# Kernel tuning notes

Measured on AMD Instinct MI355X. Metric: run time of the kernel, lower is better.

## Reference

```python
import jax, jax.numpy as jnp
import numpy as np

D_IN = 1024
D_OUT = 1024
B, S = 4, 2048

def setup_inputs() -> dict:
    key = jax.random.key(0)
    ks = jax.random.split(key, 7)
    s_in = 1.0 / np.sqrt(D_IN)
    return {
        "X": jax.random.normal(ks[0], (B, S, D_IN), dtype=jnp.float32),
        "Wq": jax.random.uniform(ks[1], (D_OUT, D_IN), jnp.float32, -s_in, s_in),
        "bq": jax.random.uniform(ks[2], (D_OUT,), jnp.float32, -s_in, s_in),
        "Wk": jax.random.uniform(ks[3], (D_OUT, D_IN), jnp.float32, -s_in, s_in),
        "bk": jax.random.uniform(ks[4], (D_OUT,), jnp.float32, -s_in, s_in),
        "Wv": jax.random.uniform(ks[5], (D_OUT, D_IN), jnp.float32, -s_in, s_in),
        "bv": jax.random.uniform(ks[6], (D_OUT,), jnp.float32, -s_in, s_in),
    }

def reference(X, Wq, bq, Wk, bk, Wv, bv):
    # Linear projections (torch Linear: x @ W.T + b)
    q = X @ Wq.T + bq            # [B, S, D_OUT]
    k = X @ Wk.T + bk
    v = X @ Wv.T + bv
    scores = jnp.einsum("bqd,bkd->bqk", q, k) / jnp.sqrt(jnp.float32(D_OUT))
    seq = scores.shape[-1]
    causal = jnp.tril(jnp.ones((seq, seq), dtype=bool))  # True where allowed
    scores = jnp.where(causal, scores, -jnp.inf)
    attn = jax.nn.softmax(scores, axis=-1)
    return jnp.einsum("bqk,bkd->bqd", attn, v)
```

## Files before the change

kernel.cpp:

```cpp
#include <hip/hip_runtime.h>
#include <hip/hip_bf16.h>
#include <hip/hip_fp8.h>


typedef __attribute__((ext_vector_type(8))) short short8;
typedef __attribute__((ext_vector_type(4))) float floatx4;
typedef __attribute__((ext_vector_type(2))) long longx2;

#define SEQ   2048
#define DMODEL 1024
#define NBATCH 4
#define MTOT  (SEQ * NBATCH)

__device__ __forceinline__ void stage16(const void* g, void* l)
{
  __builtin_amdgcn_global_load_lds(
      (const __attribute__((address_space(1))) void*)g,
      (__attribute__((address_space(3))) void*)l, 16, 0, 0);
}

__device__ __forceinline__ unsigned short bf16_bits(float f)
{
  __hip_bfloat16 h = __float2bfloat16(f);
  return *(unsigned short*)&h;
}

__device__ __forceinline__ unsigned char fp8_bits(float f)
{
  __hip_fp8_e4m3 h(f);
  return h.__x;
}

__global__ __launch_bounds__(256) void convert_all(
    const float* __restrict__ X,  const float* __restrict__ Wq,
    const float* __restrict__ Wk, const float* __restrict__ Wv,
    __hip_bfloat16* __restrict__ Xb,  __hip_bfloat16* __restrict__ Wqb,
    __hip_bfloat16* __restrict__ Wkb, __hip_bfloat16* __restrict__ Wvb)
{
  const int b = blockIdx.x;
  const float* src; __hip_bfloat16* dst; int rel;
  if (b < 8192)       { src = X;  dst = Xb;  rel = b; }
  else if (b < 9216)  { src = Wq; dst = Wqb; rel = b - 8192; }
  else if (b < 10240) { src = Wk; dst = Wkb; rel = b - 9216; }
  else                { src = Wv; dst = Wvb; rel = b - 10240; }
  const int i = rel * 1024 + threadIdx.x * 4;
  float4 f = *(const float4*)(src + i);
  uint2 o;
  o.x = (unsigned)bf16_bits(f.x) | ((unsigned)bf16_bits(f.y) << 16);
  o.y = (unsigned)bf16_bits(f.z) | ((unsigned)bf16_bits(f.w) << 16);
  *(uint2*)(dst + i) = o;
}

__global__ __launch_bounds__(256, 2) void gemm_qkv_fused(
    const __hip_bfloat16* __restrict__ Xb,
    const __hip_bfloat16* __restrict__ Wqb,
    const __hip_bfloat16* __restrict__ Wkb,
    const __hip_bfloat16* __restrict__ Wvb,
    const float* __restrict__ bq, const float* __restrict__ bk, const float* __restrict__ bv,
    unsigned char* __restrict__ Qb, unsigned char* __restrict__ Kb,
    __hip_bfloat16* __restrict__ Vt)
{
  __shared__ __hip_bfloat16 As[128 * 32];
  __shared__ __hip_bfloat16 Bs[3][128 * 32];
  const int m0 = blockIdx.y * 128, n0 = blockIdx.x * 128;
  const int tid  = threadIdx.x;
  const int lane = tid & 63;
  const int wave = tid >> 6;
  const int quad = lane >> 4;
  const int r    = lane & 15;
  const int wm   = (wave >> 1) * 64;
  const int wn   = (wave & 1) * 64;
  const int srow = wave * 16 + (lane >> 2);
  const int scol = (lane & 3) * 8;

  const __hip_bfloat16* Wp[3] = {Wqb, Wkb, Wvb};

  __hip_bfloat16* lA0 = As + wave * 512;
  __hip_bfloat16* lA1 = As + 2048 + wave * 512;

  const __hip_bfloat16* aR0 = Xb + (size_t)(m0 + srow) * DMODEL + scol;
  const __hip_bfloat16* aR1 = aR0 + (size_t)64 * DMODEL;

  floatx4 acc[3][4][4] = {};

  for (int kt = 0; kt < DMODEL / 32; ++kt) {
    const int k0 = kt * 32;
    stage16(aR0 + k0, lA0);
    stage16(aR1 + k0, lA1);
#pragma unroll
    for (int w = 0; w < 3; ++w) {
      stage16(Wp[w] + (size_t)(n0 + srow) * DMODEL + scol + k0,      Bs[w] + wave * 512);
      stage16(Wp[w] + (size_t)(n0 + 64 + srow) * DMODEL + scol + k0, Bs[w] + 2048 + wave * 512);
    }
    __syncthreads();
    short8 a[4];
#pragma unroll
    for (int i = 0; i < 4; ++i)
      a[i] = *(const short8*)(As + (wm + i * 16 + r) * 32 + quad * 8);
#pragma unroll
    for (int w = 0; w < 3; ++w) {
      short8 b[4];
#pragma unroll
      for (int j = 0; j < 4; ++j)
        b[j] = *(const short8*)(Bs[w] + (wn + j * 16 + r) * 32 + quad * 8);
#pragma unroll
      for (int i = 0; i < 4; ++i)
#pragma unroll
        for (int j = 0; j < 4; ++j)
          acc[w][i][j] = __builtin_amdgcn_mfma_f32_16x16x32_bf16(a[i], b[j], acc[w][i][j], 0, 0, 0);
    }
    __syncthreads();
  }

  {
    unsigned char* Op[2] = {Qb, Kb};
    const float* Bp[2] = {bq, bk};
#pragma unroll
    for (int w = 0; w < 2; ++w) {
      unsigned char* out = Op[w];
#pragma unroll
      for (int j = 0; j < 4; ++j) {
        const int n = n0 + wn + j * 16 + r;
        const float bb = Bp[w][n];
#pragma unroll
        for (int i = 0; i < 4; ++i) {
          const int mbase = m0 + wm + i * 16 + quad * 4;
#pragma unroll
          for (int e = 0; e < 4; ++e)
            out[(size_t)(mbase + e) * DMODEL + n] = fp8_bits(acc[w][i][j][e] + bb);
        }
      }
    }
  }
  {
    const int z    = m0 >> 11;
    const int posb = (m0 & (SEQ - 1)) + wm;
    __hip_bfloat16* vt = Vt + (size_t)z * DMODEL * SEQ;
#pragma unroll
    for (int j = 0; j < 4; ++j) {
      const int n = n0 + wn + j * 16 + r;
      const float bb = bv[n];
#pragma unroll
      for (int i = 0; i < 4; ++i) {
        const int pos = posb + i * 16 + quad * 4;
        unsigned long long pk =
            (unsigned long long)bf16_bits(acc[2][i][j][0] + bb)
          | ((unsigned long long)bf16_bits(acc[2][i][j][1] + bb) << 16)
          | ((unsigned long long)bf16_bits(acc[2][i][j][2] + bb) << 32)
          | ((unsigned long long)bf16_bits(acc[2][i][j][3] + bb) << 48);
        *(unsigned long long*)(vt + (size_t)n * SEQ + pos) = pk;
      }
    }
  }
}

__device__ __forceinline__ void gemm_core_2w_fp8(
    const unsigned char* __restrict__ A,
    const unsigned char* __restrict__ B,
    int K, int m0, int n0, int kchunks,
    unsigned char* As , unsigned char* Bs ,
    floatx4 acc[4][4])
{
  const int tid  = threadIdx.x;
  const int lane = tid & 63;
  const int wave = tid >> 6;
  const int quad = lane >> 4;
  const int r    = lane & 15;
  const int wn   = wave * 64;
  const int lrow = lane >> 2;
  const int lcol = (lane & 3) * 16;

  const unsigned char* aB = A + (size_t)(m0 + wave * 32 + lrow) * K + lcol;
  const unsigned char* bB = B + (size_t)(n0 + wave * 64 + lrow) * K + lcol;
  unsigned char* lA = As + wave * 2048;
  unsigned char* lB = Bs + wave * 4096;

  for (int kt = 0; kt < kchunks; ++kt) {
    const int k0 = kt * 64;
#pragma unroll
    for (int s = 0; s < 2; ++s)
      stage16(aB + (size_t)(16 * s) * K + k0, lA + s * 1024);
#pragma unroll
    for (int s = 0; s < 4; ++s)
      stage16(bB + (size_t)(16 * s) * K + k0, lB + s * 1024);
    __syncthreads();
    longx2 a[4], b[4];
#pragma unroll
    for (int i = 0; i < 4; ++i) {
      a[i] = __builtin_bit_cast(longx2, *(const int4*)(As + (i * 16 + r) * 64 + quad * 16));
      b[i] = __builtin_bit_cast(longx2, *(const int4*)(Bs + (wn + i * 16 + r) * 64 + quad * 16));
    }
#pragma unroll
    for (int kk = 0; kk < 2; ++kk)
#pragma unroll
      for (int i = 0; i < 4; ++i)
#pragma unroll
        for (int j = 0; j < 4; ++j)
          acc[i][j] = __builtin_amdgcn_mfma_f32_16x16x32_fp8_fp8(
              a[i][kk], b[j][kk], acc[i][j], 0, 0, 0);
    __syncthreads();
  }
}

template <bool SUMS>
__device__ __forceinline__ void gemm_core_2w(
    const __hip_bfloat16* __restrict__ A,
    const __hip_bfloat16* __restrict__ B,
    int K, int m0, int n0, int kchunks,
    __hip_bfloat16* As , __hip_bfloat16* Bs ,
    floatx4 acc[4][4], floatx4 acc_s[4])
{
  const int tid  = threadIdx.x;
  const int lane = tid & 63;
  const int wave = tid >> 6;
  const int quad = lane >> 4;
  const int r    = lane & 15;
  const int wn   = wave * 64;
  const int lrow = lane >> 2;
  const int lcol = (lane & 3) * 8;

  short8 ones;
#pragma unroll
  for (int t = 0; t < 8; ++t) ones[t] = (short)0x3F80;

  const __hip_bfloat16* aB = A + (size_t)(m0 + wave * 32 + lrow) * K + lcol;
  const __hip_bfloat16* bB = B + (size_t)(n0 + wave * 64 + lrow) * K + lcol;
  __hip_bfloat16* lA = As + wave * 1024;
  __hip_bfloat16* lB = Bs + wave * 2048;

  for (int kt = 0; kt < kchunks; ++kt) {
    const int k0 = kt * 32;
#pragma unroll
    for (int s = 0; s < 2; ++s)
      stage16(aB + (size_t)(16 * s) * K + k0, lA + s * 512);
#pragma unroll
    for (int s = 0; s < 4; ++s)
      stage16(bB + (size_t)(16 * s) * K + k0, lB + s * 512);
    __syncthreads();
    short8 a[4], b[4];
#pragma unroll
    for (int i = 0; i < 4; ++i) {
      a[i] = *(const short8*)(As + (i * 16 + r) * 32 + quad * 8);
      b[i] = *(const short8*)(Bs + (wn + i * 16 + r) * 32 + quad * 8);
    }
    if (SUMS) {
#pragma unroll
      for (int i = 0; i < 4; ++i)
        acc_s[i] = __builtin_amdgcn_mfma_f32_16x16x32_bf16(a[i], ones, acc_s[i], 0, 0, 0);
    }
#pragma unroll
    for (int i = 0; i < 4; ++i)
#pragma unroll
      for (int j = 0; j < 4; ++j)
        acc[i][j] = __builtin_amdgcn_mfma_f32_16x16x32_bf16(a[i], b[j], acc[i][j], 0, 0, 0);
    __syncthreads();
  }
}

__global__ __launch_bounds__(128, 4) void gemm_scores(
    const unsigned char* __restrict__ Qb, const unsigned char* __restrict__ Kb,
    __hip_bfloat16* __restrict__ Sb)
{
  const int z = blockIdx.y;
  const int L = blockIdx.x;
  int p = (int)((sqrtf(4.0f * (float)L + 1.0f) - 1.0f) * 0.5f);
  while ((p + 1) * (p + 2) <= L) ++p;
  while (p * (p + 1) > L) --p;
  const int o  = L - p * (p + 1);
  const int mt = 2 * p + (o > p ? 1 : 0);
  const int nt = (o > p) ? (o - p - 1) : o;
  const int m0 = mt * 64, n0 = nt * 128;

  __shared__ unsigned char As[64 * 64], Bs[128 * 64];
  const unsigned char* A = Qb + (size_t)z * SEQ * DMODEL;
  const unsigned char* B = Kb + (size_t)z * SEQ * DMODEL;
  __hip_bfloat16* outp = Sb + (size_t)z * SEQ * SEQ;
  floatx4 acc[4][4] = {};
  gemm_core_2w_fp8(A, B, DMODEL, m0, n0, DMODEL / 64, As, Bs, acc);

  const int lane = threadIdx.x & 63, wave = threadIdx.x >> 6;
  const int quad = lane >> 4, r = lane & 15;
  const int wn = wave * 64;
  const float scale = 0.03125f;
#pragma unroll
  for (int i = 0; i < 4; ++i) {
    const int mbase = m0 + i * 16 + quad * 4;
#pragma unroll
    for (int e = 0; e < 4; ++e) {
      const int row = mbase + e;
#pragma unroll
      for (int j = 0; j < 4; ++j) {
        const int n = n0 + wn + j * 16 + r;
        const float pv = (n <= row) ? __expf(acc[i][j][e] * scale) : 0.f;
        outp[(size_t)row * SEQ + n] = __float2bfloat16(pv);
      }
    }
  }
}

__global__ __launch_bounds__(128, 4) void gemm_pv(
    const __hip_bfloat16* __restrict__ Sb, const __hip_bfloat16* __restrict__ Vt,
    float* __restrict__ Out)
{
  __shared__ __hip_bfloat16 As[64 * 32], Bs[128 * 32];
  const int z = blockIdx.z;
  const int mt = (int)gridDim.y - 1 - (int)blockIdx.y;
  const int m0 = mt * 64, n0 = blockIdx.x * 128;
  const __hip_bfloat16* A = Sb + (size_t)z * SEQ * SEQ;
  const __hip_bfloat16* B = Vt + (size_t)z * DMODEL * SEQ;
  float* outp = Out + (size_t)z * SEQ * DMODEL;

  floatx4 acc[4][4] = {};
  floatx4 acc_s[4] = {};
  const int kchunks = 2 * mt + 2;
  gemm_core_2w<true>(A, B, SEQ, m0, n0, kchunks, As, Bs, acc, acc_s);

  const int lane = threadIdx.x & 63, wave = threadIdx.x >> 6;
  const int quad = lane >> 4, r = lane & 15;
  const int wn = wave * 64;
#pragma unroll
  for (int i = 0; i < 4; ++i) {
    const int mbase = m0 + i * 16 + quad * 4;
    float inv[4];
#pragma unroll
    for (int e = 0; e < 4; ++e) inv[e] = 1.f / acc_s[i][e];
#pragma unroll
    for (int j = 0; j < 4; ++j) {
      const int n = n0 + wn + j * 16 + r;
#pragma unroll
      for (int e = 0; e < 4; ++e)
        outp[(size_t)(mbase + e) * DMODEL + n] = acc[i][j][e] * inv[e];
    }
  }
}

extern "C" void kernel_launch(void* const* d_in, const int* in_sizes, int n_in,
                              void* d_out, int out_size, void* d_ws, size_t ws_size,
                              hipStream_t stream)
{
  const float* X  = (const float*)d_in[0];
  const float* Wq = (const float*)d_in[1];
  const float* bq = (const float*)d_in[2];
  const float* Wk = (const float*)d_in[3];
  const float* bk = (const float*)d_in[4];
  const float* Wv = (const float*)d_in[5];
  const float* bv = (const float*)d_in[6];
  float* Out = (float*)d_out;

  char* ws = (char*)d_ws;
  size_t off = 0;
  auto alloc = [&](size_t bytes) -> void* {
    void* p = ws + off;
    off += (bytes + 255) & ~(size_t)255;
    return p;
  };
  __hip_bfloat16* Xb  = (__hip_bfloat16*)alloc((size_t)MTOT * DMODEL * 2);
  __hip_bfloat16* Wqb = (__hip_bfloat16*)alloc((size_t)DMODEL * DMODEL * 2);
  __hip_bfloat16* Wkb = (__hip_bfloat16*)alloc((size_t)DMODEL * DMODEL * 2);
  __hip_bfloat16* Wvb = (__hip_bfloat16*)alloc((size_t)DMODEL * DMODEL * 2);
  unsigned char*  Qb  = (unsigned char*)alloc((size_t)MTOT * DMODEL);
  unsigned char*  Kb  = (unsigned char*)alloc((size_t)MTOT * DMODEL);
  __hip_bfloat16* Vt  = (__hip_bfloat16*)alloc((size_t)MTOT * DMODEL * 2);
  __hip_bfloat16* Sb  = (__hip_bfloat16*)alloc((size_t)NBATCH * SEQ * SEQ * 2);
  (void)ws_size; (void)in_sizes; (void)n_in; (void)out_size;

  convert_all<<<11264, 256, 0, stream>>>(X, Wq, Wk, Wv, Xb, Wqb, Wkb, Wvb);
  gemm_qkv_fused<<<dim3(DMODEL / 128, MTOT / 128), 256, 0, stream>>>(
      Xb, Wqb, Wkb, Wvb, bq, bk, bv, Qb, Kb, Vt);
  gemm_scores<<<dim3(272, NBATCH), 128, 0, stream>>>(Qb, Kb, Sb);
  gemm_pv<<<dim3(DMODEL / 128, SEQ / 64, NBATCH), 128, 0, stream>>>(Sb, Vt, Out);
}
```

Baseline: 235.6 us.

## Enlarge score and PV GEMM tiles to 128x128 with 4 waves and XCD-aware block mapping

The scores and PV GEMMs move from 64x128 tiles on 2 waves to 128x128 tiles on 4 waves arranged 2x2. This raises operand reuse per LDS load and halves the number of tile loads per output. Block indices are remapped so neighbouring work lands on the same XCD, which should improve L2 locality, and PV processes heavy rows first. The trade-off is coarser causal granularity, with more masked work on diagonal tiles, and fewer blocks for load balancing.

```diff
diff --git a/kernel.cpp b/kernel.cpp
--- a/kernel.cpp
+++ b/kernel.cpp
@@ -154,7 +154,7 @@
   }
 }
 
-__device__ __forceinline__ void gemm_core_2w_fp8(
+__device__ __forceinline__ void gemm_core_4w_fp8(
     const unsigned char* __restrict__ A,
     const unsigned char* __restrict__ B,
     int K, int m0, int n0, int kchunks,
@@ -166,28 +166,28 @@
   const int wave = tid >> 6;
   const int quad = lane >> 4;
   const int r    = lane & 15;
-  const int wn   = wave * 64;
+  const int wm   = (wave >> 1) * 64;
+  const int wn   = (wave & 1) * 64;
   const int lrow = lane >> 2;
   const int lcol = (lane & 3) * 16;
 
   const unsigned char* aB = A + (size_t)(m0 + wave * 32 + lrow) * K + lcol;
-  const unsigned char* bB = B + (size_t)(n0 + wave * 64 + lrow) * K + lcol;
+  const unsigned char* bB = B + (size_t)(n0 + wave * 32 + lrow) * K + lcol;
   unsigned char* lA = As + wave * 2048;
-  unsigned char* lB = Bs + wave * 4096;
+  unsigned char* lB = Bs + wave * 2048;
 
   for (int kt = 0; kt < kchunks; ++kt) {
     const int k0 = kt * 64;
 #pragma unroll
-    for (int s = 0; s < 2; ++s)
+    for (int s = 0; s < 2; ++s) {
       stage16(aB + (size_t)(16 * s) * K + k0, lA + s * 1024);
-#pragma unroll
-    for (int s = 0; s < 4; ++s)
       stage16(bB + (size_t)(16 * s) * K + k0, lB + s * 1024);
+    }
     __syncthreads();
     longx2 a[4], b[4];
 #pragma unroll
     for (int i = 0; i < 4; ++i) {
-      a[i] = __builtin_bit_cast(longx2, *(const int4*)(As + (i * 16 + r) * 64 + quad * 16));
+      a[i] = __builtin_bit_cast(longx2, *(const int4*)(As + (wm + i * 16 + r) * 64 + quad * 16));
       b[i] = __builtin_bit_cast(longx2, *(const int4*)(Bs + (wn + i * 16 + r) * 64 + quad * 16));
     }
 #pragma unroll
@@ -203,7 +203,7 @@
 }
 
 template <bool SUMS>
-__device__ __forceinline__ void gemm_core_2w(
+__device__ __forceinline__ void gemm_core_4w(
     const __hip_bfloat16* __restrict__ A,
     const __hip_bfloat16* __restrict__ B,
     int K, int m0, int n0, int kchunks,
@@ -215,7 +215,8 @@
   const int wave = tid >> 6;
   const int quad = lane >> 4;
   const int r    = lane & 15;
-  const int wn   = wave * 64;
+  const int wm   = (wave >> 1) * 64;
+  const int wn   = (wave & 1) * 64;
   const int lrow = lane >> 2;
   const int lcol = (lane & 3) * 8;
 
@@ -224,23 +225,22 @@
   for (int t = 0; t < 8; ++t) ones[t] = (short)0x3F80;
 
   const __hip_bfloat16* aB = A + (size_t)(m0 + wave * 32 + lrow) * K + lcol;
-  const __hip_bfloat16* bB = B + (size_t)(n0 + wave * 64 + lrow) * K + lcol;
+  const __hip_bfloat16* bB = B + (size_t)(n0 + wave * 32 + lrow) * K + lcol;
   __hip_bfloat16* lA = As + wave * 1024;
-  __hip_bfloat16* lB = Bs + wave * 2048;
+  __hip_bfloat16* lB = Bs + wave * 1024;
 
   for (int kt = 0; kt < kchunks; ++kt) {
     const int k0 = kt * 32;
 #pragma unroll
-    for (int s = 0; s < 2; ++s)
+    for (int s = 0; s < 2; ++s) {
       stage16(aB + (size_t)(16 * s) * K + k0, lA + s * 512);
-#pragma unroll
-    for (int s = 0; s < 4; ++s)
       stage16(bB + (size_t)(16 * s) * K + k0, lB + s * 512);
+    }
     __syncthreads();
     short8 a[4], b[4];
 #pragma unroll
     for (int i = 0; i < 4; ++i) {
-      a[i] = *(const short8*)(As + (i * 16 + r) * 32 + quad * 8);
+      a[i] = *(const short8*)(As + (wm + i * 16 + r) * 32 + quad * 8);
       b[i] = *(const short8*)(Bs + (wn + i * 16 + r) * 32 + quad * 8);
     }
     if (SUMS) {
@@ -257,34 +257,35 @@
   }
 }
 
-__global__ __launch_bounds__(128, 4) void gemm_scores(
+__global__ __launch_bounds__(256, 2) void gemm_scores(
     const unsigned char* __restrict__ Qb, const unsigned char* __restrict__ Kb,
     __hip_bfloat16* __restrict__ Sb)
 {
-  const int z = blockIdx.y;
-  const int L = blockIdx.x;
-  int p = (int)((sqrtf(4.0f * (float)L + 1.0f) - 1.0f) * 0.5f);
-  while ((p + 1) * (p + 2) <= L) ++p;
-  while (p * (p + 1) > L) --p;
-  const int o  = L - p * (p + 1);
-  const int mt = 2 * p + (o > p ? 1 : 0);
-  const int nt = (o > p) ? (o - p - 1) : o;
-  const int m0 = mt * 64, n0 = nt * 128;
-
-  __shared__ unsigned char As[64 * 64], Bs[128 * 64];
+  const int b    = blockIdx.x;
+  const int orig = (b & 7) * 68 + (b >> 3);
+  const int z    = orig / 136;
+  const int L    = orig - z * 136;
+  int mt = (int)((sqrtf(8.0f * (float)L + 1.0f) - 1.0f) * 0.5f);
+  while ((mt + 1) * (mt + 2) / 2 <= L) ++mt;
+  while (mt * (mt + 1) / 2 > L) --mt;
+  const int nt = L - mt * (mt + 1) / 2;
+  const int m0 = mt * 128, n0 = nt * 128;
+
+  __shared__ __align__(16) unsigned char As[128 * 64];
+  __shared__ __align__(16) unsigned char Bs[128 * 64];
   const unsigned char* A = Qb + (size_t)z * SEQ * DMODEL;
   const unsigned char* B = Kb + (size_t)z * SEQ * DMODEL;
   __hip_bfloat16* outp = Sb + (size_t)z * SEQ * SEQ;
   floatx4 acc[4][4] = {};
-  gemm_core_2w_fp8(A, B, DMODEL, m0, n0, DMODEL / 64, As, Bs, acc);
+  gemm_core_4w_fp8(A, B, DMODEL, m0, n0, DMODEL / 64, As, Bs, acc);
 
   const int lane = threadIdx.x & 63, wave = threadIdx.x >> 6;
   const int quad = lane >> 4, r = lane & 15;
-  const int wn = wave * 64;
+  const int wm = (wave >> 1) * 64, wn = (wave & 1) * 64;
   const float scale = 0.03125f;
 #pragma unroll
   for (int i = 0; i < 4; ++i) {
-    const int mbase = m0 + i * 16 + quad * 4;
+    const int mbase = m0 + wm + i * 16 + quad * 4;
 #pragma unroll
     for (int e = 0; e < 4; ++e) {
       const int row = mbase + e;
@@ -298,29 +299,37 @@
   }
 }
 
-__global__ __launch_bounds__(128, 4) void gemm_pv(
+__global__ __launch_bounds__(256, 2) void gemm_pv(
     const __hip_bfloat16* __restrict__ Sb, const __hip_bfloat16* __restrict__ Vt,
     float* __restrict__ Out)
 {
-  __shared__ __hip_bfloat16 As[64 * 32], Bs[128 * 32];
-  const int z = blockIdx.z;
-  const int mt = (int)gridDim.y - 1 - (int)blockIdx.y;
-  const int m0 = mt * 64, n0 = blockIdx.x * 128;
+  const int b    = blockIdx.x;
+  const int xcd  = b & 7;
+  const int slot = b >> 3;
+  const int gi   = slot >> 3;
+  const int q    = gi * 8 + xcd;
+  const int n0   = (slot & 7) * 128;
+  const int z    = q & 3;
+  const int mt   = 15 - (q >> 2);
+  const int m0   = mt * 128;
+
+  __shared__ __align__(16) __hip_bfloat16 As[128 * 32];
+  __shared__ __align__(16) __hip_bfloat16 Bs[128 * 32];
   const __hip_bfloat16* A = Sb + (size_t)z * SEQ * SEQ;
   const __hip_bfloat16* B = Vt + (size_t)z * DMODEL * SEQ;
   float* outp = Out + (size_t)z * SEQ * DMODEL;
 
   floatx4 acc[4][4] = {};
   floatx4 acc_s[4] = {};
-  const int kchunks = 2 * mt + 2;
-  gemm_core_2w<true>(A, B, SEQ, m0, n0, kchunks, As, Bs, acc, acc_s);
+  const int kchunks = 4 * mt + 4;
+  gemm_core_4w<true>(A, B, SEQ, m0, n0, kchunks, As, Bs, acc, acc_s);
 
   const int lane = threadIdx.x & 63, wave = threadIdx.x >> 6;
   const int quad = lane >> 4, r = lane & 15;
-  const int wn = wave * 64;
+  const int wm = (wave >> 1) * 64, wn = (wave & 1) * 64;
 #pragma unroll
   for (int i = 0; i < 4; ++i) {
-    const int mbase = m0 + i * 16 + quad * 4;
+    const int mbase = m0 + wm + i * 16 + quad * 4;
     float inv[4];
 #pragma unroll
     for (int e = 0; e < 4; ++e) inv[e] = 1.f / acc_s[i][e];
@@ -367,6 +376,6 @@
   convert_all<<<11264, 256, 0, stream>>>(X, Wq, Wk, Wv, Xb, Wqb, Wkb, Wvb);
   gemm_qkv_fused<<<dim3(DMODEL / 128, MTOT / 128), 256, 0, stream>>>(
       Xb, Wqb, Wkb, Wvb, bq, bk, bv, Qb, Kb, Vt);
-  gemm_scores<<<dim3(272, NBATCH), 128, 0, stream>>>(Qb, Kb, Sb);
-  gemm_pv<<<dim3(DMODEL / 128, SEQ / 64, NBATCH), 128, 0, stream>>>(Sb, Vt, Out);
-}
+  gemm_scores<<<dim3(544), 256, 0, stream>>>(Qb, Kb, Sb);
+  gemm_pv<<<dim3(512), 256, 0, stream>>>(Sb, Vt, Out);
+}
```

Result: faster. 219.0 us (-7.1%).
